# Kernel optimization log

Measured on AMD Instinct MI355X. Metric: run time of the kernel, lower is better.

The kernel has to match this reference:

```python
import jax, jax.numpy as jnp
import numpy as np
from jax import lax

BIG = 1e10  # initial distance, matching torch's 1e10


def farthest_point_sample(xyz, init_farthest, npoint):
    """xyz: [B,N,3] float; init_farthest: [B] int32; returns centroids [B,npoint] int32."""
    B, N, _ = xyz.shape
    batch_idx = jnp.arange(B)

    def body(i, state):
        centroids, distance, farthest = state
        centroids = centroids.at[:, i].set(farthest)
        c = xyz[batch_idx, farthest][:, None, :]              # [B,1,3] current centroid
        dist = jnp.sum(jnp.square(xyz - c), axis=-1)          # [B,N] sq. distance
        distance = jnp.minimum(distance, dist)                # mask-update: keep min dist to any centroid
        farthest = jnp.argmax(distance, axis=-1).astype(jnp.int32)
        return centroids, distance, farthest

    centroids0 = jnp.zeros((B, npoint), jnp.int32)
    distance0 = jnp.full((B, N), BIG, xyz.dtype)
    centroids, _, _ = lax.fori_loop(0, npoint, body, (centroids0, distance0, init_farthest.astype(jnp.int32)))
    return centroids


def setup_inputs() -> dict:
    key = jax.random.key(0)
    k1, k2, k3 = jax.random.split(key, 3)
    B, N = 16, 100000
    mesh = jax.random.normal(k1, (B, N, 3), dtype=jnp.float32)
    contact_map = jax.random.uniform(k2, (B, N, 1), dtype=jnp.float32)
    init_farthest = jax.random.randint(k3, (B,), 0, N, dtype=jnp.int32)
    return {"mesh": mesh, "contact_map": contact_map, "init_farthest": init_farthest, "npoint": 1024}


def reference(mesh, contact_map, init_farthest, npoint):
    B, N, _ = mesh.shape
    batch_idx = jnp.arange(B)

    # __compute_mesh_scale: max distance from centroid, per batch
    centroid = jnp.mean(mesh, axis=1, keepdims=True)                      # [B,1,3]
    s_obj = jnp.max(jnp.sqrt(jnp.sum(jnp.square(mesh - centroid), axis=2)), axis=1)  # [B]

    # __farthest_point_sample
    centroids = farthest_point_sample(mesh, init_farthest, npoint)        # [B,npoint]

    # gather sampled points and contact values
    point_cloud = mesh[batch_idx[:, None], centroids]                     # [B,npoint,3]
    cm_sampled = contact_map[batch_idx[:, None], centroids]               # [B,npoint,1]

    # normalize by object scale (broadcast over points/coords)
    point_cloud_norm = point_cloud / s_obj[:, None, None]

    # point_cloud_norm_contact fed to the contact encoder in the original
    return jnp.concatenate([cm_sampled, point_cloud_norm], axis=2)        # [B,npoint,4]
```

## Files before the change

### kernel.cpp

```cpp
#include <hip/hip_runtime.h>
#include <cstdint>

#define NBATCH 16
#define NPTS   100000
#define NPOINT 1024
#define GPB    16
#define TPB    256
#define STRIDE (GPB * TPB)
#define KPT    25


__global__ __launch_bounds__(256) void sum_kernel(const float* __restrict__ xyz,
                                                  float* __restrict__ sums) {
    const int b   = blockIdx.x & 15;
    const int sub = blockIdx.x >> 4;
    const float* P = xyz + (size_t)b * NPTS * 3;
    float sx = 0.f, sy = 0.f, sz = 0.f;
    for (int i = sub * TPB + threadIdx.x; i < NPTS; i += 8 * TPB) {
        sx += P[i * 3 + 0];
        sy += P[i * 3 + 1];
        sz += P[i * 3 + 2];
    }
    #pragma unroll
    for (int off = 32; off; off >>= 1) {
        sx += __shfl_xor(sx, off);
        sy += __shfl_xor(sy, off);
        sz += __shfl_xor(sz, off);
    }
    __shared__ float r[3][4];
    const int wave = threadIdx.x >> 6, lane = threadIdx.x & 63;
    if (lane == 0) { r[0][wave] = sx; r[1][wave] = sy; r[2][wave] = sz; }
    __syncthreads();
    if (threadIdx.x == 0) {
        atomicAdd(&sums[b * 4 + 0], r[0][0] + r[0][1] + r[0][2] + r[0][3]);
        atomicAdd(&sums[b * 4 + 1], r[1][0] + r[1][1] + r[1][2] + r[1][3]);
        atomicAdd(&sums[b * 4 + 2], r[2][0] + r[2][1] + r[2][2] + r[2][3]);
    }
}

__global__ __launch_bounds__(256) void max_kernel(const float* __restrict__ xyz,
                                                  const float* __restrict__ sums,
                                                  unsigned* __restrict__ maxbits) {
    const int b   = blockIdx.x & 15;
    const int sub = blockIdx.x >> 4;
    const float* P = xyz + (size_t)b * NPTS * 3;
    const float mx = sums[b * 4 + 0] / (float)NPTS;
    const float my = sums[b * 4 + 1] / (float)NPTS;
    const float mz = sums[b * 4 + 2] / (float)NPTS;
    float best = 0.f;
    for (int i = sub * TPB + threadIdx.x; i < NPTS; i += 8 * TPB) {
        float dx = P[i * 3 + 0] - mx;
        float dy = P[i * 3 + 1] - my;
        float dz = P[i * 3 + 2] - mz;
        float d = dx * dx + dy * dy + dz * dz;
        best = fmaxf(best, d);
    }
    #pragma unroll
    for (int off = 32; off; off >>= 1) best = fmaxf(best, __shfl_xor(best, off));
    __shared__ float r[4];
    const int wave = threadIdx.x >> 6, lane = threadIdx.x & 63;
    if (lane == 0) r[wave] = best;
    __syncthreads();
    if (threadIdx.x == 0) {
        float m = fmaxf(fmaxf(r[0], r[1]), fmaxf(r[2], r[3]));
        atomicMax(&maxbits[b], __float_as_uint(m));
    }
}

__global__ __launch_bounds__(256) void fps_kernel(const float* __restrict__ xyz,
                                                  const float* __restrict__ cmap,
                                                  const int* __restrict__ init_far,
                                                  const unsigned* __restrict__ maxbits,
                                                  unsigned long long* __restrict__ slots,
                                                  float* __restrict__ out) {
    const int b   = blockIdx.x & 15;
    const int g   = blockIdx.x >> 4;
    const int tid = threadIdx.x;
    const int tl  = g * TPB + tid;
    const float* P = xyz + (size_t)b * NPTS * 3;

    float px[KPT], py[KPT], pz[KPT], pd[KPT];
    #pragma unroll
    for (int k = 0; k < KPT; ++k) {
        const int p = tl + k * STRIDE;
        const bool v = p < NPTS;
        px[k] = v ? P[p * 3 + 0] : 0.f;
        py[k] = v ? P[p * 3 + 1] : 0.f;
        pz[k] = v ? P[p * 3 + 2] : 0.f;
        pd[k] = v ? 1e10f : -1.0f;
    }

    __shared__ unsigned long long lds_key[4];
    __shared__ int lds_win;
    const int wave = tid >> 6, lane = tid & 63;

    int cur = init_far[b];
    const float sb = sqrtf(__uint_as_float(maxbits[b]));
    const bool writer = (g == 0) && (tid == 0);

    for (int i = 0; i < NPOINT; ++i) {
        const float cx = P[cur * 3 + 0];
        const float cy = P[cur * 3 + 1];
        const float cz = P[cur * 3 + 2];

        if (writer) {
            const float c = cmap[(size_t)b * NPTS + cur];
            float* o = out + ((size_t)b * NPOINT + i) * 4;
            o[0] = c;
            o[1] = cx / sb;
            o[2] = cy / sb;
            o[3] = cz / sb;
        }
        if (i == NPOINT - 1) break;

        float best = -1.0f;
        int bestk = 0;
        {
            #pragma clang fp contract(off)
            #pragma unroll
            for (int k = 0; k < KPT; ++k) {
                float dx = px[k] - cx;
                float dy = py[k] - cy;
                float dz = pz[k] - cz;
                float dist = dx * dx + dy * dy;
                dist = dist + dz * dz;
                float nd = fminf(pd[k], dist);
                pd[k] = nd;
                if (nd > best) { best = nd; bestk = k; }
            }
        }
        const unsigned pidx = (unsigned)(tl + bestk * STRIDE);
        unsigned long long key =
            ((unsigned long long)__float_as_uint(best) << 22) |
            (unsigned long long)(0x3FFFFFu - pidx);

        #pragma unroll
        for (int off = 32; off; off >>= 1) {
            unsigned long long o2 = __shfl_xor(key, off);
            key = o2 > key ? o2 : key;
        }
        if (lane == 0) lds_key[wave] = key;
        __syncthreads();

        if (wave == 0) {
            unsigned long long kb = lds_key[0];
            kb = lds_key[1] > kb ? lds_key[1] : kb;
            kb = lds_key[2] > kb ? lds_key[2] : kb;
            kb = lds_key[3] > kb ? lds_key[3] : kb;
            const unsigned long long send = kb | ((unsigned long long)(i + 1) << 54);
            if (lane == 0)
                __hip_atomic_store(&slots[(i & 1) * 256 + b * GPB + g], send,
                                   __ATOMIC_RELAXED, __HIP_MEMORY_SCOPE_AGENT);
            unsigned long long v = 0;
            if (lane < GPB) {
                unsigned long long* sp = &slots[(i & 1) * 256 + b * GPB + lane];
                const unsigned long long want = (unsigned long long)(i + 1);
                for (;;) {
                    v = __hip_atomic_load(sp, __ATOMIC_RELAXED, __HIP_MEMORY_SCOPE_AGENT);
                    if ((v >> 54) >= want) break;
                    __builtin_amdgcn_s_sleep(1);
                }
            }
            #pragma unroll
            for (int off = 8; off; off >>= 1) {
                unsigned long long o2 = __shfl_xor(v, off);
                v = o2 > v ? o2 : v;
            }
            if (lane == 0)
                lds_win = (int)(0x3FFFFFu - (unsigned)(v & 0x3FFFFFu));
        }
        __syncthreads();
        cur = lds_win;
    }
}

extern "C" void kernel_launch(void* const* d_in, const int* in_sizes, int n_in,
                              void* d_out, int out_size, void* d_ws, size_t ws_size,
                              hipStream_t stream) {
    const float* mesh = (const float*)d_in[0];
    const float* cmap = (const float*)d_in[1];
    const int* init   = (const int*)d_in[2];
    float* out = (float*)d_out;

    char* ws = (char*)d_ws;
    float* sums                 = (float*)ws;
    unsigned* maxbits           = (unsigned*)(ws + 256);
    unsigned long long* slots   = (unsigned long long*)(ws + 4096);

    hipMemsetAsync(d_ws, 0, 8192, stream);
    sum_kernel<<<dim3(128), dim3(TPB), 0, stream>>>(mesh, sums);
    max_kernel<<<dim3(128), dim3(TPB), 0, stream>>>(mesh, sums, maxbits);
    fps_kernel<<<dim3(256), dim3(TPB), 0, stream>>>(mesh, cmap, init, maxbits, slots, out);
}
```

Baseline: 2.402 ms.

## Publish per-wave keys to global slots and drop block barriers in FPS loop

```diff
diff --git a/kernel.cpp b/kernel.cpp
--- a/kernel.cpp
+++ b/kernel.cpp
@@ -6,6 +6,8 @@
 #define NPOINT 1024
 #define GPB    16
 #define TPB    256
+#define WPB    4
+#define NSLOT  (GPB * WPB)
 #define STRIDE (GPB * TPB)
 #define KPT    25
 
@@ -90,9 +92,10 @@
         pd[k] = v ? 1e10f : -1.0f;
     }
 
-    __shared__ unsigned long long lds_key[4];
-    __shared__ int lds_win;
     const int wave = tid >> 6, lane = tid & 63;
+    const int myslot = g * WPB + wave;
+    unsigned long long* const batch_slots0 = slots + (size_t)b * NSLOT;
+    unsigned long long* const batch_slots1 = slots + 1024 + (size_t)b * NSLOT;
 
     int cur = init_far[b];
     const float sb = sqrtf(__uint_as_float(maxbits[b]));
@@ -139,38 +142,30 @@
             unsigned long long o2 = __shfl_xor(key, off);
             key = o2 > key ? o2 : key;
         }
-        if (lane == 0) lds_key[wave] = key;
-        __syncthreads();
 
-        if (wave == 0) {
-            unsigned long long kb = lds_key[0];
-            kb = lds_key[1] > kb ? lds_key[1] : kb;
-            kb = lds_key[2] > kb ? lds_key[2] : kb;
-            kb = lds_key[3] > kb ? lds_key[3] : kb;
-            const unsigned long long send = kb | ((unsigned long long)(i + 1) << 54);
-            if (lane == 0)
-                __hip_atomic_store(&slots[(i & 1) * 256 + b * GPB + g], send,
-                                   __ATOMIC_RELAXED, __HIP_MEMORY_SCOPE_AGENT);
-            unsigned long long v = 0;
-            if (lane < GPB) {
-                unsigned long long* sp = &slots[(i & 1) * 256 + b * GPB + lane];
-                const unsigned long long want = (unsigned long long)(i + 1);
-                for (;;) {
-                    v = __hip_atomic_load(sp, __ATOMIC_RELAXED, __HIP_MEMORY_SCOPE_AGENT);
-                    if ((v >> 54) >= want) break;
-                    __builtin_amdgcn_s_sleep(1);
-                }
+        const unsigned long long want = (unsigned long long)(i + 1);
+        unsigned long long* const bs = (i & 1) ? batch_slots1 : batch_slots0;
+
+        if (lane == 0)
+            __hip_atomic_store(&bs[myslot], key | (want << 54),
+                               __ATOMIC_RELAXED, __HIP_MEMORY_SCOPE_AGENT);
+
+        unsigned long long v;
+        {
+            unsigned long long* sp = &bs[lane];
+            int tries = 0;
+            for (;;) {
+                v = __hip_atomic_load(sp, __ATOMIC_RELAXED, __HIP_MEMORY_SCOPE_AGENT);
+                if ((v >> 54) >= want) break;
+                if (++tries > 48) __builtin_amdgcn_s_sleep(1);
             }
-            #pragma unroll
-            for (int off = 8; off; off >>= 1) {
-                unsigned long long o2 = __shfl_xor(v, off);
-                v = o2 > v ? o2 : v;
-            }
-            if (lane == 0)
-                lds_win = (int)(0x3FFFFFu - (unsigned)(v & 0x3FFFFFu));
         }
-        __syncthreads();
-        cur = lds_win;
+        #pragma unroll
+        for (int off = 32; off; off >>= 1) {
+            unsigned long long o2 = __shfl_xor(v, off);
+            v = o2 > v ? o2 : v;
+        }
+        cur = (int)(0x3FFFFFu - (unsigned)(v & 0x3FFFFFu));
     }
 }
 
@@ -183,11 +178,11 @@
     float* out = (float*)d_out;
 
     char* ws = (char*)d_ws;
-    float* sums                 = (float*)ws;
-    unsigned* maxbits           = (unsigned*)(ws + 256);
-    unsigned long long* slots   = (unsigned long long*)(ws + 4096);
+    float* sums               = (float*)ws;
+    unsigned* maxbits         = (unsigned*)(ws + 256);
+    unsigned long long* slots = (unsigned long long*)(ws + 4096);
 
-    hipMemsetAsync(d_ws, 0, 8192, stream);
+    hipMemsetAsync(d_ws, 0, 20480, stream);
     sum_kernel<<<dim3(128), dim3(TPB), 0, stream>>>(mesh, sums);
     max_kernel<<<dim3(128), dim3(TPB), 0, stream>>>(mesh, sums, maxbits);
     fps_kernel<<<dim3(256), dim3(TPB), 0, stream>>>(mesh, cmap, init, maxbits, slots, out);
```

Measured after the change: 6.104 ms. 154% more time.

## Remove memset and atomics, prefetch centroid, spin before sleeping in FPS barrier

Applied to the files above, without the earlier changes.

```diff
diff --git a/kernel.cpp b/kernel.cpp
--- a/kernel.cpp
+++ b/kernel.cpp
@@ -6,17 +6,22 @@
 #define NPOINT 1024
 #define GPB    16
 #define TPB    256
+#define WPB    4
+#define NSUB   16
 #define STRIDE (GPB * TPB)
 #define KPT    25
+#define NPAIR  13
+
+typedef unsigned long long u64;
 
 
 __global__ __launch_bounds__(256) void sum_kernel(const float* __restrict__ xyz,
-                                                  float* __restrict__ sums) {
+                                                  float* __restrict__ psum) {
     const int b   = blockIdx.x & 15;
     const int sub = blockIdx.x >> 4;
     const float* P = xyz + (size_t)b * NPTS * 3;
     float sx = 0.f, sy = 0.f, sz = 0.f;
-    for (int i = sub * TPB + threadIdx.x; i < NPTS; i += 8 * TPB) {
+    for (int i = sub * TPB + threadIdx.x; i < NPTS; i += NSUB * TPB) {
         sx += P[i * 3 + 0];
         sy += P[i * 3 + 1];
         sz += P[i * 3 + 2];
@@ -32,28 +37,38 @@
     if (lane == 0) { r[0][wave] = sx; r[1][wave] = sy; r[2][wave] = sz; }
     __syncthreads();
     if (threadIdx.x == 0) {
-        atomicAdd(&sums[b * 4 + 0], r[0][0] + r[0][1] + r[0][2] + r[0][3]);
-        atomicAdd(&sums[b * 4 + 1], r[1][0] + r[1][1] + r[1][2] + r[1][3]);
-        atomicAdd(&sums[b * 4 + 2], r[2][0] + r[2][1] + r[2][2] + r[2][3]);
+        float* o = psum + (b * NSUB + sub) * 4;
+        o[0] = r[0][0] + r[0][1] + r[0][2] + r[0][3];
+        o[1] = r[1][0] + r[1][1] + r[1][2] + r[1][3];
+        o[2] = r[2][0] + r[2][1] + r[2][2] + r[2][3];
     }
 }
 
 __global__ __launch_bounds__(256) void max_kernel(const float* __restrict__ xyz,
-                                                  const float* __restrict__ sums,
-                                                  unsigned* __restrict__ maxbits) {
+                                                  const float* __restrict__ psum,
+                                                  unsigned* __restrict__ pmax,
+                                                  u64* __restrict__ slots) {
+    if (blockIdx.x == 0) {
+        slots[threadIdx.x] = 0ull;
+        slots[threadIdx.x + 256] = 0ull;
+    }
     const int b   = blockIdx.x & 15;
     const int sub = blockIdx.x >> 4;
     const float* P = xyz + (size_t)b * NPTS * 3;
-    const float mx = sums[b * 4 + 0] / (float)NPTS;
-    const float my = sums[b * 4 + 1] / (float)NPTS;
-    const float mz = sums[b * 4 + 2] / (float)NPTS;
+    float sx = 0.f, sy = 0.f, sz = 0.f;
+    #pragma unroll
+    for (int s = 0; s < NSUB; ++s) {
+        sx += psum[(b * NSUB + s) * 4 + 0];
+        sy += psum[(b * NSUB + s) * 4 + 1];
+        sz += psum[(b * NSUB + s) * 4 + 2];
+    }
+    const float mx = sx / (float)NPTS, my = sy / (float)NPTS, mz = sz / (float)NPTS;
     float best = 0.f;
-    for (int i = sub * TPB + threadIdx.x; i < NPTS; i += 8 * TPB) {
+    for (int i = sub * TPB + threadIdx.x; i < NPTS; i += NSUB * TPB) {
         float dx = P[i * 3 + 0] - mx;
         float dy = P[i * 3 + 1] - my;
         float dz = P[i * 3 + 2] - mz;
-        float d = dx * dx + dy * dy + dz * dz;
-        best = fmaxf(best, d);
+        best = fmaxf(best, dx * dx + dy * dy + dz * dz);
     }
     #pragma unroll
     for (int off = 32; off; off >>= 1) best = fmaxf(best, __shfl_xor(best, off));
@@ -61,116 +76,126 @@
     const int wave = threadIdx.x >> 6, lane = threadIdx.x & 63;
     if (lane == 0) r[wave] = best;
     __syncthreads();
-    if (threadIdx.x == 0) {
-        float m = fmaxf(fmaxf(r[0], r[1]), fmaxf(r[2], r[3]));
-        atomicMax(&maxbits[b], __float_as_uint(m));
-    }
-}
-
-__global__ __launch_bounds__(256) void fps_kernel(const float* __restrict__ xyz,
-                                                  const float* __restrict__ cmap,
-                                                  const int* __restrict__ init_far,
-                                                  const unsigned* __restrict__ maxbits,
-                                                  unsigned long long* __restrict__ slots,
-                                                  float* __restrict__ out) {
+    if (threadIdx.x == 0)
+        pmax[b * NSUB + sub] = __float_as_uint(fmaxf(fmaxf(r[0], r[1]), fmaxf(r[2], r[3])));
+}
+
+__global__ __launch_bounds__(256, 1) void fps_kernel(const float* __restrict__ xyz,
+                                                     const float* __restrict__ cmap,
+                                                     const int* __restrict__ init_far,
+                                                     const unsigned* __restrict__ pmax,
+                                                     u64* __restrict__ slots,
+                                                     float* __restrict__ out) {
     const int b   = blockIdx.x & 15;
     const int g   = blockIdx.x >> 4;
     const int tid = threadIdx.x;
+    const int wave = tid >> 6, lane = tid & 63;
     const int tl  = g * TPB + tid;
     const float* P = xyz + (size_t)b * NPTS * 3;
 
-    float px[KPT], py[KPT], pz[KPT], pd[KPT];
-    #pragma unroll
-    for (int k = 0; k < KPT; ++k) {
-        const int p = tl + k * STRIDE;
-        const bool v = p < NPTS;
-        px[k] = v ? P[p * 3 + 0] : 0.f;
-        py[k] = v ? P[p * 3 + 1] : 0.f;
-        pz[k] = v ? P[p * 3 + 2] : 0.f;
-        pd[k] = v ? 1e10f : -1.0f;
-    }
-
-    __shared__ unsigned long long lds_key[4];
+    float m = 0.f;
+    #pragma unroll
+    for (int s = 0; s < NSUB; ++s) m = fmaxf(m, __uint_as_float(pmax[b * NSUB + s]));
+    const float sb = sqrtf(m);
+
+    float pxx[NPAIR], pxy[NPAIR], pyx[NPAIR], pyy[NPAIR],
+          pzx[NPAIR], pzy[NPAIR], pdx[NPAIR], pdy[NPAIR];
+    #pragma unroll
+    for (int j = 0; j < NPAIR; ++j) {
+        const int p0 = tl + (2 * j) * STRIDE;
+        const int p1 = tl + (2 * j + 1) * STRIDE;
+        const bool v0 = p0 < NPTS, v1 = p1 < NPTS;
+        pxx[j] = v0 ? P[p0 * 3 + 0] : 0.f;  pxy[j] = v1 ? P[p1 * 3 + 0] : 0.f;
+        pyx[j] = v0 ? P[p0 * 3 + 1] : 0.f;  pyy[j] = v1 ? P[p1 * 3 + 1] : 0.f;
+        pzx[j] = v0 ? P[p0 * 3 + 2] : 0.f;  pzy[j] = v1 ? P[p1 * 3 + 2] : 0.f;
+        pdx[j] = v0 ? 1e10f : -1.0f;        pdy[j] = v1 ? 1e10f : -1.0f;
+    }
+
+    __shared__ u64 lds_key[WPB];
     __shared__ int lds_win;
-    const int wave = tid >> 6, lane = tid & 63;
 
     int cur = init_far[b];
-    const float sb = sqrtf(__uint_as_float(maxbits[b]));
-    const bool writer = (g == 0) && (tid == 0);
+    float cx = P[cur * 3 + 0], cy = P[cur * 3 + 1], cz = P[cur * 3 + 2];
+    const bool wrblk = (g == 0);
 
     for (int i = 0; i < NPOINT; ++i) {
-        const float cx = P[cur * 3 + 0];
-        const float cy = P[cur * 3 + 1];
-        const float cz = P[cur * 3 + 2];
-
-        if (writer) {
-            const float c = cmap[(size_t)b * NPTS + cur];
-            float* o = out + ((size_t)b * NPOINT + i) * 4;
-            o[0] = c;
-            o[1] = cx / sb;
-            o[2] = cy / sb;
-            o[3] = cz / sb;
-        }
-        if (i == NPOINT - 1) break;
+        if (i == NPOINT - 1) {
+            if (wrblk && tid == 64) {
+                float* o = out + ((size_t)b * NPOINT + i) * 4;
+                o[0] = cmap[(size_t)b * NPTS + cur];
+                o[1] = cx / sb; o[2] = cy / sb; o[3] = cz / sb;
+            }
+            break;
+        }
 
         float best = -1.0f;
-        int bestk = 0;
+        int bidx = 0;
         {
             #pragma clang fp contract(off)
             #pragma unroll
-            for (int k = 0; k < KPT; ++k) {
-                float dx = px[k] - cx;
-                float dy = py[k] - cy;
-                float dz = pz[k] - cz;
-                float dist = dx * dx + dy * dy;
-                dist = dist + dz * dz;
-                float nd = fminf(pd[k], dist);
-                pd[k] = nd;
-                if (nd > best) { best = nd; bestk = k; }
-            }
-        }
-        const unsigned pidx = (unsigned)(tl + bestk * STRIDE);
-        unsigned long long key =
-            ((unsigned long long)__float_as_uint(best) << 22) |
-            (unsigned long long)(0x3FFFFFu - pidx);
-
+            for (int j = 0; j < NPAIR; ++j) {
+                float dx0 = pxx[j] - cx, dx1 = pxy[j] - cx;
+                float dy0 = pyx[j] - cy, dy1 = pyy[j] - cy;
+                float dz0 = pzx[j] - cz, dz1 = pzy[j] - cz;
+                float s0 = dx0 * dx0 + dy0 * dy0;  float s1 = dx1 * dx1 + dy1 * dy1;
+                s0 = s0 + dz0 * dz0;               s1 = s1 + dz1 * dz1;
+                float n0 = fminf(pdx[j], s0);      float n1 = fminf(pdy[j], s1);
+                pdx[j] = n0;                       pdy[j] = n1;
+                if (n0 > best) { best = n0; bidx = tl + (2 * j) * STRIDE; }
+                if (n1 > best) { best = n1; bidx = tl + (2 * j + 1) * STRIDE; }
+            }
+        }
+
+        const u64 want = (u64)(i + 1);
+        u64 key = ((u64)__float_as_uint(best) << 22) | (u64)(0x3FFFFFu - (unsigned)bidx);
         #pragma unroll
         for (int off = 32; off; off >>= 1) {
-            unsigned long long o2 = __shfl_xor(key, off);
+            u64 o2 = __shfl_xor(key, off);
             key = o2 > key ? o2 : key;
         }
         if (lane == 0) lds_key[wave] = key;
         __syncthreads();
 
+        u64* const bs = slots + ((size_t)(i & 1) * NBATCH + b) * GPB;
+
         if (wave == 0) {
-            unsigned long long kb = lds_key[0];
-            kb = lds_key[1] > kb ? lds_key[1] : kb;
-            kb = lds_key[2] > kb ? lds_key[2] : kb;
-            kb = lds_key[3] > kb ? lds_key[3] : kb;
-            const unsigned long long send = kb | ((unsigned long long)(i + 1) << 54);
+            u64 bk = (lane < WPB) ? lds_key[lane] : 0;
+            #pragma unroll
+            for (int off = 1; off < WPB; off <<= 1) {
+                u64 o2 = __shfl_xor(bk, off);
+                bk = o2 > bk ? o2 : bk;
+            }
             if (lane == 0)
-                __hip_atomic_store(&slots[(i & 1) * 256 + b * GPB + g], send,
+                __hip_atomic_store(&bs[g], bk | (want << 54),
                                    __ATOMIC_RELAXED, __HIP_MEMORY_SCOPE_AGENT);
-            unsigned long long v = 0;
+
+            u64 v = 0;
             if (lane < GPB) {
-                unsigned long long* sp = &slots[(i & 1) * 256 + b * GPB + lane];
-                const unsigned long long want = (unsigned long long)(i + 1);
+                u64* sp = &bs[lane];
+                int tries = 0;
                 for (;;) {
                     v = __hip_atomic_load(sp, __ATOMIC_RELAXED, __HIP_MEMORY_SCOPE_AGENT);
                     if ((v >> 54) >= want) break;
-                    __builtin_amdgcn_s_sleep(1);
+                    if (++tries > 16) __builtin_amdgcn_s_sleep(1);
                 }
             }
             #pragma unroll
             for (int off = 8; off; off >>= 1) {
-                unsigned long long o2 = __shfl_xor(v, off);
+                u64 o2 = __shfl_xor(v, off);
                 v = o2 > v ? o2 : v;
             }
             if (lane == 0)
                 lds_win = (int)(0x3FFFFFu - (unsigned)(v & 0x3FFFFFu));
+        } else if (wave == 1 && wrblk && lane == 0) {
+            float* o = out + ((size_t)b * NPOINT + i) * 4;
+            o[0] = cmap[(size_t)b * NPTS + cur];
+            o[1] = cx / sb; o[2] = cy / sb; o[3] = cz / sb;
         }
         __syncthreads();
         cur = lds_win;
+        cx = P[cur * 3 + 0];
+        cy = P[cur * 3 + 1];
+        cz = P[cur * 3 + 2];
     }
 }
 
@@ -182,13 +207,12 @@
     const int* init   = (const int*)d_in[2];
     float* out = (float*)d_out;
 
-    char* ws = (char*)d_ws;
-    float* sums                 = (float*)ws;
-    unsigned* maxbits           = (unsigned*)(ws + 256);
-    unsigned long long* slots   = (unsigned long long*)(ws + 4096);
-
-    hipMemsetAsync(d_ws, 0, 8192, stream);
-    sum_kernel<<<dim3(128), dim3(TPB), 0, stream>>>(mesh, sums);
-    max_kernel<<<dim3(128), dim3(TPB), 0, stream>>>(mesh, sums, maxbits);
-    fps_kernel<<<dim3(256), dim3(TPB), 0, stream>>>(mesh, cmap, init, maxbits, slots, out);
-}
+    char* ws      = (char*)d_ws;
+    float* psum   = (float*)ws;
+    unsigned* pmx = (unsigned*)(ws + 4096);
+    u64* slots    = (u64*)(ws + 8192);
+
+    sum_kernel<<<dim3(256), dim3(TPB), 0, stream>>>(mesh, psum);
+    max_kernel<<<dim3(256), dim3(TPB), 0, stream>>>(mesh, psum, pmx, slots);
+    fps_kernel<<<dim3(256), dim3(TPB), 0, stream>>>(mesh, cmap, init, pmx, slots, out);
+}
```

Measured after the change: 2.004 ms. 1.2x faster.
